# Kernel optimization log

Measured on AMD Instinct MI355X. Metric: run time of the kernel, lower is better.

## Reference

```python
import jax, jax.numpy as jnp
import numpy as np

# Model dims: batch, seq, d_model, heads, layers, vocab, ffn, max_distance
B, S, D, H, L, V, F, M = 2, 1024, 1024, 16, 6, 32000, 4096, 1024
Dh = D // H


def setup_inputs() -> dict:
    key = jax.random.key(0)
    ks = jax.random.split(key, 24)
    std = 0.02
    w = lambda k, shape: (jax.random.normal(k, shape, jnp.float32) * std)
    return {
        "tokens": jax.random.randint(ks[0], (B, S), 0, V, jnp.int32),
        "emb": w(ks[1], (V, D)),
        "Wq": w(ks[2], (L, D, D)), "bq": jnp.zeros((L, D), jnp.float32),
        "Wk": w(ks[3], (L, D, D)), "bk": jnp.zeros((L, D), jnp.float32),
        "Wv": w(ks[4], (L, D, D)), "bv": jnp.zeros((L, D), jnp.float32),
        "Wo": w(ks[5], (L, D, D)), "bo": jnp.zeros((L, D), jnp.float32),
        "rpe": w(ks[6], (L, M, Dh)),  # per-layer key-RPE embedding table
        "ln1_s": jnp.ones((L, D), jnp.float32), "ln1_b": jnp.zeros((L, D), jnp.float32),
        "ln2_s": jnp.ones((L, D), jnp.float32), "ln2_b": jnp.zeros((L, D), jnp.float32),
        "W1": w(ks[7], (L, D, F)), "b1": jnp.zeros((L, F), jnp.float32),
        "W2": w(ks[8], (L, F, D)), "b2": jnp.zeros((L, D), jnp.float32),
        "Wout": w(ks[9], (D, V)), "bout": jnp.zeros((V,), jnp.float32),
    }


def _ln(x, s, b):
    mu = jnp.mean(x, -1, keepdims=True)
    var = jnp.mean((x - mu) ** 2, -1, keepdims=True)
    return (x - mu) * jax.lax.rsqrt(var + 1e-5) * s + b


def _forward(tokens, emb, Wq, bq, Wk, bk, Wv, bv, Wo, bo, rpe,
             ln1_s, ln1_b, ln2_s, ln2_b, W1, b1, W2, b2, Wout, bout):
    x = emb[tokens]  # (B, S, D); dropout is identity at inference
    mask = jnp.tril(jnp.ones((S, S), bool))
    inv_sqrt_d = np.float32(1.0 / np.sqrt(Dh))

    def block(x, p):
        (wq, bq_, wk, bk_, wv, bv_, wo, bo_, rp,
         l1s, l1b, l2s, l2b, w1, b1_, w2, b2_) = p
        heads = lambda W, b: (x @ W + b).reshape(B, S, H, Dh).transpose(0, 2, 1, 3)
        q, k, v = heads(wq, bq_), heads(wk, bk_), heads(wv, bv_)
        qk = jnp.einsum('bhqd,bhkd->bhqk', q, k)
        # Music-Transformer skew: srel = Q @ E^T, pad-left 1, reshape, drop first row
        srel = jnp.einsum('bhqd,md->bhqm', q, rp[-S:])  # M == S, no clipping branch
        srel = jnp.pad(srel, ((0, 0), (0, 0), (0, 0), (1, 0)))
        srel = srel.reshape(B, H, S + 1, S)[:, :, 1:, :]
        logits = (qk + srel) * inv_sqrt_d
        logits = jnp.where(mask, logits, jnp.float32(-1e9))
        wgt = jax.nn.softmax(logits, axis=-1)
        o = jnp.einsum('bhqk,bhkd->bhqd', wgt, v).transpose(0, 2, 1, 3).reshape(B, S, D)
        o = o @ wo + bo_
        x2 = _ln(x + o, l1s, l1b)           # post-LN residual (attention)
        f = jax.nn.gelu(x2 @ w1 + b1_) @ w2 + b2_
        return _ln(x2 + f, l2s, l2b), None  # post-LN residual (FFN)

    x, _ = jax.lax.scan(block, x, (Wq, bq, Wk, bk, Wv, bv, Wo, bo, rpe,
                                   ln1_s, ln1_b, ln2_s, ln2_b, W1, b1, W2, b2))
    return x @ Wout + bout  # (B, S, V)


def reference(tokens, emb, Wq, bq, Wk, bk, Wv, bv, Wo, bo, rpe,
              ln1_s, ln1_b, ln2_s, ln2_b, W1, b1, W2, b2, Wout, bout):
    return _forward(tokens, emb, Wq, bq, Wk, bk, Wv, bv, Wo, bo, rpe,
                    ln1_s, ln1_b, ln2_s, ln2_b, W1, b1, W2, b2, Wout, bout)
```

## Files before the change

kernel.cpp:

```cpp
#include <hip/hip_runtime.h>
#include <hip/hip_bf16.h>
#include <cstdint>

constexpr int NB = 2, NS = 1024, ND = 1024, NH = 16, NL = 6, NV = 32000, NF = 4096, NDH = 64;

using bf16 = __hip_bfloat16;
typedef __bf16 bf16x8 __attribute__((ext_vector_type(8)));
typedef float f32x4 __attribute__((ext_vector_type(4)));

#define AS1(p) ((const __attribute__((address_space(1))) void*)(p))
#define AS3(p) ((__attribute__((address_space(3))) void*)(p))

__device__ __forceinline__ float gelu_f(float x) {
  float z = 1.5957691216057308f * (x + 0.044715f * x * x * x);
  return x / (1.f + __expf(-z));
}

template<int EP, bool HASBIAS>
__global__ __launch_bounds__(512)
void gemm256p(const bf16* __restrict__ A, const bf16* __restrict__ Bt,
              void* __restrict__ Cv, const float* __restrict__ bias,
              int K, int lda, int ldb, int ldc)
{
  const int nM = gridDim.y, nN = gridDim.x;
  const int nwg = nM * nN;
  const int bid = blockIdx.y * nN + blockIdx.x;
  const int wg = (bid & 7) * (nwg >> 3) + (bid >> 3);
  const int m0 = (wg % nM) * 256;
  const int n0 = (wg / nM) * 256;

  __shared__ char lds[131072];

  const int tid = threadIdx.x, lane = tid & 63, wid = tid >> 6;
  const int wm = (wid >> 2) * 128;
  const int wn = (wid & 3) * 64;
  const int l15 = lane & 15, g4 = lane >> 4;
  const int rdk = (g4 * 16) ^ ((l15 >> 3) << 5);

  const int srow = wid * 16 + (lane >> 2);
  const int scol = ((lane & 3) * 8) ^ (((lane >> 5) & 1) << 4);
  const bf16* gA = A  + (long)(m0 + srow) * lda + scol;
  const bf16* gB = Bt + (long)(n0 + srow) * ldb + scol;
  const long a128 = 128l * lda, b128 = 128l * ldb;

  f32x4 acc[8][4] = {};
  const int NP = K >> 5;

#define STGP(p_) do {                                                                  \
    const int s_ = (p_) & 3; const long ko_ = (long)(p_) * 32;                         \
    char* dA = lds + s_ * 32768 + wid * 1024;                                          \
    char* dB = dA + 16384;                                                             \
    __builtin_amdgcn_global_load_lds(AS1(gA + ko_),        AS3(dA),        16, 0, 0);  \
    __builtin_amdgcn_global_load_lds(AS1(gA + ko_ + a128), AS3(dA + 8192), 16, 0, 0);  \
    __builtin_amdgcn_global_load_lds(AS1(gB + ko_),        AS3(dB),        16, 0, 0);  \
    __builtin_amdgcn_global_load_lds(AS1(gB + ko_ + b128), AS3(dB + 8192), 16, 0, 0);  \
  } while (0)

#define PAIR(vm_, p_, DOSTG_) do {                                                     \
    asm volatile("s_waitcnt vmcnt(" #vm_ ")" ::: "memory");                            \
    __builtin_amdgcn_s_barrier();                                                      \
    asm volatile("" ::: "memory");                                                     \
    const char* la_ = lds + ((p_) & 3) * 32768;                                        \
    const char* lb_ = la_ + 16384;                                                     \
    bf16x8 bfr[4], af[8];                                                              \
    _Pragma("unroll") for (int j_ = 0; j_ < 4; ++j_)                                   \
      bfr[j_] = *(const bf16x8*)(lb_ + (wn + j_ * 16 + l15) * 64 + rdk);               \
    _Pragma("unroll") for (int i_ = 0; i_ < 4; ++i_)                                   \
      af[i_] = *(const bf16x8*)(la_ + (wm + i_ * 16 + l15) * 64 + rdk);                \
    __builtin_amdgcn_sched_barrier(0);                                                 \
    _Pragma("unroll") for (int i_ = 4; i_ < 8; ++i_)                                   \
      af[i_] = *(const bf16x8*)(la_ + (wm + i_ * 16 + l15) * 64 + rdk);                \
    if (DOSTG_) STGP((p_) + 3);                                                        \
    asm volatile("s_waitcnt lgkmcnt(4)" ::: "memory");                                 \
    __builtin_amdgcn_sched_barrier(0);                                                 \
    __builtin_amdgcn_s_setprio(1);                                                     \
    _Pragma("unroll") for (int i_ = 0; i_ < 4; ++i_)                                   \
      _Pragma("unroll") for (int j_ = 0; j_ < 4; ++j_)                                 \
        acc[i_][j_] = __builtin_amdgcn_mfma_f32_16x16x32_bf16(af[i_], bfr[j_], acc[i_][j_], 0, 0, 0); \
    __builtin_amdgcn_s_setprio(0);                                                     \
    asm volatile("s_waitcnt lgkmcnt(0)" ::: "memory");                                 \
    __builtin_amdgcn_sched_barrier(0);                                                 \
    __builtin_amdgcn_s_setprio(1);                                                     \
    _Pragma("unroll") for (int i_ = 4; i_ < 8; ++i_)                                   \
      _Pragma("unroll") for (int j_ = 0; j_ < 4; ++j_)                                 \
        acc[i_][j_] = __builtin_amdgcn_mfma_f32_16x16x32_bf16(af[i_], bfr[j_], acc[i_][j_], 0, 0, 0); \
    __builtin_amdgcn_s_setprio(0);                                                     \
  } while (0)

  STGP(0); STGP(1); STGP(2);
  for (int p = 0; p < NP - 3; ++p) PAIR(8, p, 1);
  PAIR(8, NP - 3, 0);
  PAIR(4, NP - 2, 0);
  PAIR(0, NP - 1, 0);
#undef PAIR
#undef STGP

  const int rq = (lane >> 4) * 4;
  #pragma unroll
  for (int i = 0; i < 8; ++i) {
    const int r0 = m0 + wm + i * 16 + rq;
    #pragma unroll
    for (int j = 0; j < 4; ++j) {
      const int c = n0 + wn + j * 16 + l15;
      float bv = 0.f;
      if constexpr (HASBIAS) bv = bias[c];
      #pragma unroll
      for (int e = 0; e < 4; ++e) {
        float v = acc[i][j][e] + bv;
        if constexpr (EP == 2) v = gelu_f(v);
        if constexpr (EP == 0) ((float*)Cv)[(long)(r0 + e) * ldc + c] = v;
        else                   ((bf16*)Cv)[(long)(r0 + e) * ldc + c] = __float2bfloat16(v);
      }
    }
  }
}

template<int EP, bool HASBIAS, int KSZ>
__global__ __launch_bounds__(256)
void gemm128_bt(const bf16* __restrict__ A, const bf16* __restrict__ Bt,
                void* __restrict__ Cv, const float* __restrict__ bias,
                int K, int lda, int ldb, int ldc, long sEP)
{
  const int nM = gridDim.y, nN = gridDim.x;
  const int nwg = nM * nN;
  const int bid = blockIdx.y * nN + blockIdx.x;
  const int qq = nwg >> 3;
  const int wg = (bid & 7) * qq + (bid >> 3);
  const int m0 = (wg % nM) * 128;
  const int n0 = (wg / nM) * 256;

  const int kLen = K / KSZ;
  const long kOff = (long)blockIdx.z * kLen;

  __shared__ char lds[73728];

  const int tid  = threadIdx.x;
  const int lane = tid & 63;
  const int wid  = tid >> 6;
  const int wn   = wid * 64;
  const int l15  = lane & 15;
  const int rdk  = ((lane >> 4) * 16) ^ ((l15 >> 3) << 5);

  const int srow = wid * 16 + (lane >> 2);
  const int scol = ((lane & 3) * 8) ^ (((lane >> 5) & 1) << 4);
  const bf16* gA = A  + (long)(m0 + srow) * lda + scol + kOff;
  const bf16* gB = Bt + (long)(n0 + srow) * ldb + scol + kOff;
  const long a64 = 64l * lda, b64 = 64l * ldb;

  f32x4 acc[8][4] = {};
  const int NT = kLen >> 5;

#define STG(t_, b_) do {                                                               \
    char* dA = lds + (b_) * 24576 + wid * 1024;                                        \
    char* dB = lds + (b_) * 24576 + 8192 + wid * 1024;                                 \
    const long ko_ = (long)(t_) * 32;                                                  \
    __builtin_amdgcn_global_load_lds(AS1(gA + ko_),           AS3(dA),         16, 0, 0); \
    __builtin_amdgcn_global_load_lds(AS1(gA + ko_ + a64),     AS3(dA + 4096),  16, 0, 0); \
    __builtin_amdgcn_global_load_lds(AS1(gB + ko_),           AS3(dB),         16, 0, 0); \
    __builtin_amdgcn_global_load_lds(AS1(gB + ko_ + b64),     AS3(dB + 4096),  16, 0, 0); \
    __builtin_amdgcn_global_load_lds(AS1(gB + ko_ + 2 * b64), AS3(dB + 8192),  16, 0, 0); \
    __builtin_amdgcn_global_load_lds(AS1(gB + ko_ + 3 * b64), AS3(dB + 12288), 16, 0, 0); \
  } while (0)

#define TBODY(cur_) do {                                                               \
    const char* la_ = lds + (cur_) * 24576;                                            \
    const char* lb_ = la_ + 8192;                                                      \
    bf16x8 bf_[4], af_[8];                                                             \
    _Pragma("unroll") for (int j_ = 0; j_ < 4; ++j_)                                   \
      bf_[j_] = *(const bf16x8*)(lb_ + (wn + j_ * 16 + l15) * 64 + rdk);               \
    _Pragma("unroll") for (int i_ = 0; i_ < 8; ++i_)                                   \
      af_[i_] = *(const bf16x8*)(la_ + (i_ * 16 + l15) * 64 + rdk);                    \
    __builtin_amdgcn_s_setprio(1);                                                     \
    _Pragma("unroll") for (int i_ = 0; i_ < 8; ++i_)                                   \
      _Pragma("unroll") for (int j_ = 0; j_ < 4; ++j_)                                 \
        acc[i_][j_] = __builtin_amdgcn_mfma_f32_16x16x32_bf16(af_[i_], bf_[j_], acc[i_][j_], 0, 0, 0); \
    __builtin_amdgcn_s_setprio(0);                                                     \
  } while (0)

  STG(0, 0); STG(1, 1);
  int cur = 0, nxt = 2;
  for (int t = 0; t < NT - 1; ++t) {
    asm volatile("s_waitcnt vmcnt(6)" ::: "memory");
    __builtin_amdgcn_s_barrier();
    asm volatile("" ::: "memory");
    if (t + 2 < NT) STG(t + 2, nxt);
    TBODY(cur);
    cur = (cur == 2) ? 0 : cur + 1;
    nxt = (nxt == 2) ? 0 : nxt + 1;
  }
  asm volatile("s_waitcnt vmcnt(0)" ::: "memory");
  __builtin_amdgcn_s_barrier();
  asm volatile("" ::: "memory");
  TBODY(cur);
#undef TBODY
#undef STG

  const int rq = (lane >> 4) * 4;
  #pragma unroll
  for (int i = 0; i < 8; ++i) {
    const int r0 = m0 + i * 16 + rq;
    #pragma unroll
    for (int j = 0; j < 4; ++j) {
      const int c = n0 + wn + j * 16 + l15;
      float bv = 0.f;
      if constexpr (HASBIAS) { if (KSZ == 1 || blockIdx.z == 0) bv = bias[c]; }
      #pragma unroll
      for (int e = 0; e < 4; ++e) {
        float v = acc[i][j][e] + bv;
        if constexpr (EP == 0) {
          float* Cz = (float*)Cv + (KSZ > 1 ? (long)blockIdx.z * sEP : 0);
          Cz[(long)(r0 + e) * ldc + c] = v;
        } else if constexpr (EP == 2) {
          ((bf16*)Cv)[(long)(r0 + e) * ldc + c] = __float2bfloat16(gelu_f(v));
        } else {
          ((bf16*)Cv)[(long)(c >> 10) * sEP + (long)(r0 + e) * ND + (c & 1023)] =
              __float2bfloat16(v);
        }
      }
    }
  }
}

template<int BN, int EP, int CZ, bool HASBIAS, int SWZ, int KS>
__global__ __launch_bounds__(256)
void gemm_bt(const bf16* __restrict__ A, const bf16* __restrict__ Bt,
             void* __restrict__ Cv, const float* __restrict__ bias,
             int M, int N, int K, int lda, int ldb, int ldc, int ZH,
             long sAb, long sAh, long sBb, long sBh, long sCb, long sCh, long sBias)
{
  constexpr int BM = 128, BK = 32;
  constexpr int WGN = (BN == 128) ? 2 : 1;
  constexpr int FM  = (BM / (4 / WGN)) / 16;
  constexpr int FN  = (BN / WGN) / 16;

  const int z  = blockIdx.z;
  const int zb = z / ZH, zh = z % ZH;
  const bf16* Ab = A + (long)zb * sAb + (long)zh * sAh;
  const bf16* Bb = Bt + (long)zb * sBb + (long)zh * sBh;

  const int m0 = blockIdx.y * BM;
  const int n0 = blockIdx.x * BN;

  if constexpr (CZ == 3) { if (m0 + n0 + BM + BN - 2 < NS - 1) return; }

  __shared__ bf16 Asm[BM * BK];
  __shared__ bf16 Bsm[BN * BK];

  const int tid  = threadIdx.x;
  const int lane = tid & 63;
  const int wid  = tid >> 6;
  const int wm = (wid / WGN) * (FM * 16);
  const int wn = (wid % WGN) * (FN * 16);
  const int l15 = lane & 15;
  const int lk8 = (lane >> 4) * 8;

  f32x4 acc[FM][FN] = {};

  const int srow = tid >> 2;
  const int scol = (tid & 3) * 8;
  const bf16* gA = Ab + (long)(m0 + srow) * lda + scol;
  const bf16* gB = Bb + (long)(n0 + srow) * ldb + scol;
  bf16* ldsA = Asm + wid * 512;
  bf16* ldsB = Bsm + wid * 512;

  for (int k0 = 0; k0 < K; k0 += BK) {
    __builtin_amdgcn_global_load_lds(AS1(gA + k0), AS3(ldsA), 16, 0, 0);
    __builtin_amdgcn_global_load_lds(AS1(gA + 64l * lda + k0), AS3(ldsA + 2048), 16, 0, 0);
    __builtin_amdgcn_global_load_lds(AS1(gB + k0), AS3(ldsB), 16, 0, 0);
    if constexpr (BN == 128)
      __builtin_amdgcn_global_load_lds(AS1(gB + 64l * ldb + k0), AS3(ldsB + 2048), 16, 0, 0);
    asm volatile("s_waitcnt vmcnt(0)" ::: "memory");
    __syncthreads();

    bf16x8 af[FM], bfr[FN];
    #pragma unroll
    for (int i = 0; i < FM; ++i)
      af[i] = *reinterpret_cast<const bf16x8*>(&Asm[(wm + i * 16 + l15) * BK + lk8]);
    #pragma unroll
    for (int j = 0; j < FN; ++j)
      bfr[j] = *reinterpret_cast<const bf16x8*>(&Bsm[(wn + j * 16 + l15) * BK + lk8]);
    #pragma unroll
    for (int i = 0; i < FM; ++i)
      #pragma unroll
      for (int j = 0; j < FN; ++j)
        acc[i][j] = __builtin_amdgcn_mfma_f32_16x16x32_bf16(af[i], bfr[j], acc[i][j], 0, 0, 0);
    __syncthreads();
  }

  const int rq = (lane >> 4) * 4;
  const long cb = (long)zb * sCb + (long)zh * sCh;
  #pragma unroll
  for (int i = 0; i < FM; ++i) {
    const int r0 = m0 + wm + i * 16 + rq;
    #pragma unroll
    for (int j = 0; j < FN; ++j) {
      const int c = n0 + wn + j * 16 + l15;
      float bv = 0.f;
      if constexpr (HASBIAS) bv = bias[(long)zb * sBias + c];
      #pragma unroll
      for (int e = 0; e < 4; ++e) {
        float v = acc[i][j][e] + bv;
        const long idx = cb + (long)(r0 + e) * ldc + c;
        if constexpr (EP == 0) ((float*)Cv)[idx] = v;
        else                   ((bf16*)Cv)[idx] = __float2bfloat16(v);
      }
    }
  }
}

__global__ __launch_bounds__(256)
void flash_attn_k(const bf16* __restrict__ qkv, const bf16* __restrict__ vt,
                  const bf16* __restrict__ qe, bf16* __restrict__ ob)
{
  const int z  = blockIdx.x;
  const int qt = 15 - blockIdx.y;
  const int b  = z >> 4, h = z & 15;
  const int q0 = qt * 64;
  const int tid  = threadIdx.x;
  const int lane = tid & 63;
  const int wid  = tid >> 6;
  const int l15  = lane & 15;
  const int g4   = lane >> 4;
  const int xk   = (l15 & 7) << 4;

  __shared__ char lds[50176];
  char* Klds = lds;
  char* Vlds = lds + 16384;
  char* Plds = lds + 32768;

  const bf16* Kg  = qkv + (long)NB * NS * ND + (long)b * NS * ND + h * 64;
  const bf16* Vg  = vt + (long)z * 64 * NS;
  const bf16* QEg = qe + (long)z * NS * NS;

  const bf16* Qrow = qkv + ((long)b * NS + q0 + wid * 16 + l15) * ND + h * 64 + g4 * 8;
  const bf16x8 qr0 = *(const bf16x8*)(Qrow);
  const bf16x8 qr1 = *(const bf16x8*)(Qrow + 32);

  const int kR = tid >> 3, kSeg = tid & 7;
  const int vD = tid >> 4, vSeg = tid & 15;
  int wKa[4], wVa[4];
  #pragma unroll
  for (int i = 0; i < 4; ++i) {
    const int r = i * 32 + kR;
    wKa[i] = (r * 128 + kSeg * 16) ^ ((r & 7) << 4);
    const int d = i * 16 + vD;
    wVa[i] = (d * 256 + vSeg * 16) ^ ((d & 7) << 4);
  }

  f32x4 aqk[8], apv[4];
  #pragma unroll
  for (int j = 0; j < 4; ++j) apv[j] = (f32x4){0.f, 0.f, 0.f, 0.f};
  float mrun[4] = {-3e38f, -3e38f, -3e38f, -3e38f};
  float lrun[4] = {0.f, 0.f, 0.f, 0.f};

  const int nk = (q0 + 191) >> 7;

  bf16x8 kr[4], vr[4];
  #pragma unroll
  for (int i = 0; i < 4; ++i) {
    kr[i] = *(const bf16x8*)(Kg + (long)(i * 32 + kR) * ND + kSeg * 8);
    vr[i] = *(const bf16x8*)(Vg + (long)(i * 16 + vD) * NS + vSeg * 8);
  }

  for (int kt = 0; kt < nk; ++kt) {
    const int k0 = kt * 128;
    __builtin_amdgcn_s_barrier();

    #pragma unroll
    for (int i = 0; i < 4; ++i) *(bf16x8*)(Klds + wKa[i]) = kr[i];
    #pragma unroll
    for (int i = 0; i < 4; ++i) *(bf16x8*)(Vlds + wVa[i]) = vr[i];

    unsigned short se[4][8];
    #pragma unroll
    for (int e = 0; e < 4; ++e) {
      const int qg = q0 + wid * 16 + g4 * 4 + e;
      const long rowb = (long)qg * NS;
      #pragma unroll
      for (int f = 0; f < 8; ++f) {
        int m = 1023 - qg + k0 + 16 * f + l15;
        m = m > 1023 ? 1023 : m;
        se[e][f] = *(const unsigned short*)(QEg + rowb + m);
      }
    }
    __builtin_amdgcn_sched_barrier(0);
    if (kt + 1 < nk) {
      const int k1 = k0 + 128;
      #pragma unroll
      for (int i = 0; i < 4; ++i) {
        kr[i] = *(const bf16x8*)(Kg + (long)(k1 + i * 32 + kR) * ND + kSeg * 8);
        vr[i] = *(const bf16x8*)(Vg + (long)(i * 16 + vD) * NS + k1 + vSeg * 8);
      }
    }
    asm volatile("s_waitcnt lgkmcnt(0)" ::: "memory");
    __builtin_amdgcn_sched_barrier(0);
    __builtin_amdgcn_s_barrier();

    #pragma unroll
    for (int f = 0; f < 8; ++f) aqk[f] = (f32x4){0.f, 0.f, 0.f, 0.f};
    {
      const int ko0 = g4 * 16;
      #pragma unroll
      for (int f = 0; f < 8; ++f) {
        bf16x8 bb = *(const bf16x8*)(Klds + (((16 * f + l15) * 128 + ko0) ^ xk));
        aqk[f] = __builtin_amdgcn_mfma_f32_16x16x32_bf16(qr0, bb, aqk[f], 0, 0, 0);
      }
      const int ko1 = 64 + g4 * 16;
      #pragma unroll
      for (int f = 0; f < 8; ++f) {
        bf16x8 bb = *(const bf16x8*)(Klds + (((16 * f + l15) * 128 + ko1) ^ xk));
        aqk[f] = __builtin_amdgcn_mfma_f32_16x16x32_bf16(qr1, bb, aqk[f], 0, 0, 0);
      }
    }

    float ps[4][8];
    float scl[4];
    #pragma unroll
    for (int e = 0; e < 4; ++e) {
      const int qg = q0 + wid * 16 + g4 * 4 + e;
      float s[8];
      float mx = mrun[e];
      #pragma unroll
      for (int f = 0; f < 8; ++f) {
        const int kg = k0 + 16 * f + l15;
        const float sv = __uint_as_float((unsigned)se[e][f] << 16);
        const float t = (aqk[f][e] + sv) * 0.125f;
        s[f] = (kg <= qg) ? t : -1e30f;
        mx = fmaxf(mx, s[f]);
      }
      #pragma unroll
      for (int o = 1; o < 16; o <<= 1) mx = fmaxf(mx, __shfl_xor(mx, o));
      const float sc_ = __expf(mrun[e] - mx);
      float ls = 0.f;
      #pragma unroll
      for (int f = 0; f < 8; ++f) { const float p = __expf(s[f] - mx); ps[e][f] = p; ls += p; }
      #pragma unroll
      for (int o = 1; o < 16; o <<= 1) ls += __shfl_xor(ls, o);
      lrun[e] = lrun[e] * sc_ + ls;
      mrun[e] = mx;
      scl[e] = sc_;
    }
    #pragma unroll
    for (int fd = 0; fd < 4; ++fd)
      #pragma unroll
      for (int e = 0; e < 4; ++e) apv[fd][e] *= scl[e];

    #pragma unroll
    for (int e = 0; e < 4; ++e) {
      char* pr = Plds + (wid * 16 + g4 * 4 + e) * 272 + l15 * 2;
      #pragma unroll
      for (int f = 0; f < 8; ++f)
        *(bf16*)(pr + f * 32) = __float2bfloat16(ps[e][f]);
    }
    asm volatile("s_waitcnt lgkmcnt(0)" ::: "memory");
    __builtin_amdgcn_sched_barrier(0);

    #pragma unroll
    for (int ks = 0; ks < 4; ++ks) {
      const int ko = (ks * 32 + g4 * 8) * 2;
      bf16x8 a = *(const bf16x8*)(Plds + (wid * 16 + l15) * 272 + ko);
      #pragma unroll
      for (int fd = 0; fd < 4; ++fd) {
        bf16x8 bb = *(const bf16x8*)(Vlds + (((16 * fd + l15) * 256 + ko) ^ xk));
        apv[fd] = __builtin_amdgcn_mfma_f32_16x16x32_bf16(a, bb, apv[fd], 0, 0, 0);
      }
    }
  }

  #pragma unroll
  for (int e = 0; e < 4; ++e) {
    const float rl = 1.f / lrun[e];
    const int qg = q0 + wid * 16 + g4 * 4 + e;
    bf16* orow = ob + ((long)b * NS + qg) * ND + h * 64;
    #pragma unroll
    for (int fd = 0; fd < 4; ++fd)
      orow[16 * fd + l15] = __float2bfloat16(apv[fd][e] * rl);
  }
}

__global__ void transpose64_k(const float* __restrict__ in, bf16* __restrict__ out,
                              int R, int C, long inZ, long outZ) {
  __shared__ float t[64][65];
  const float* ip = in + (long)blockIdx.z * inZ;
  bf16* op = out + (long)blockIdx.z * outZ;
  const int c0 = blockIdx.x * 64, r0 = blockIdx.y * 64;
  const int tid = threadIdx.x;
  const int lr = tid >> 4;
  const int lc = (tid & 15) * 4;
  #pragma unroll
  for (int i = 0; i < 4; ++i) {
    const float4 v = *(const float4*)(ip + (long)(r0 + lr + 16 * i) * C + c0 + lc);
    t[lr + 16 * i][lc]     = v.x;
    t[lr + 16 * i][lc + 1] = v.y;
    t[lr + 16 * i][lc + 2] = v.z;
    t[lr + 16 * i][lc + 3] = v.w;
  }
  __syncthreads();
  #pragma unroll
  for (int i = 0; i < 4; ++i) {
    const int oc = lr + 16 * i;
    ushort4 u;
    bf16 h0 = __float2bfloat16(t[lc][oc]);
    bf16 h1 = __float2bfloat16(t[lc + 1][oc]);
    bf16 h2 = __float2bfloat16(t[lc + 2][oc]);
    bf16 h3 = __float2bfloat16(t[lc + 3][oc]);
    u.x = *(unsigned short*)&h0; u.y = *(unsigned short*)&h1;
    u.z = *(unsigned short*)&h2; u.w = *(unsigned short*)&h3;
    *(ushort4*)(op + (long)(c0 + oc) * R + r0 + lc) = u;
  }
}

__global__ void transpose_v_k(const bf16* __restrict__ v, bf16* __restrict__ vt) {
  __shared__ bf16 t[32][33];
  const int z = blockIdx.z, b = z >> 4, h = z & 15;
  const bf16* ip = v + (long)b * NS * ND + h * 64;
  bf16* op = vt + (long)z * 64 * NS;
  const int s0 = blockIdx.x * 32, d0 = blockIdx.y * 32;
  const int tx = threadIdx.x, ty = threadIdx.y;
  #pragma unroll
  for (int i = 0; i < 4; ++i)
    t[ty * 4 + i][tx] = ip[(long)(s0 + ty * 4 + i) * ND + d0 + tx];
  __syncthreads();
  #pragma unroll
  for (int i = 0; i < 4; ++i)
    op[(long)(d0 + ty * 4 + i) * NS + s0 + tx] = t[tx][ty * 4 + i];
}

__global__ void cvt_bf16_k(const float* __restrict__ in, bf16* __restrict__ out, int n) {
  int i = blockIdx.x * 256 + threadIdx.x;
  if (i < n) out[i] = __float2bfloat16(in[i]);
}

__global__ void pack3_k(const float* __restrict__ a, const float* __restrict__ b,
                        const float* __restrict__ c, float* __restrict__ out) {
  int i = blockIdx.x * 256 + threadIdx.x;
  if (i >= NL * 3 * ND) return;
  int d = i % ND, r = (i / ND) % 3, l = i / (3 * ND);
  const float* src = (r == 0) ? a : ((r == 1) ? b : c);
  out[i] = src[l * ND + d];
}

__global__ void embed_k(const int* __restrict__ tok, const float* __restrict__ emb,
                        float* __restrict__ x, bf16* __restrict__ xb) {
  const int row = blockIdx.x;
  const int t = tok[row];
  const float4 val = ((const float4*)(emb + (long)t * ND))[threadIdx.x];
  ((float4*)(x + (long)row * ND))[threadIdx.x] = val;
  bf16* xp = xb + (long)row * ND + threadIdx.x * 4;
  xp[0] = __float2bfloat16(val.x); xp[1] = __float2bfloat16(val.y);
  xp[2] = __float2bfloat16(val.z); xp[3] = __float2bfloat16(val.w);
}

__global__ void resid_ln_k(float* __restrict__ x, const float* __restrict__ g,
                           long gs,
                           const float* __restrict__ s, const float* __restrict__ b,
                           bf16* __restrict__ xb) {
  const int row = blockIdx.x, tid = threadIdx.x;
  const float4 xv = ((const float4*)(x + (long)row * ND))[tid];
  const float4 ga = ((const float4*)(g + (long)row * ND))[tid];
  const float4 gb = ((const float4*)(g + gs + (long)row * ND))[tid];
  const float4 gc = ((const float4*)(g + 2 * gs + (long)row * ND))[tid];
  const float4 gd = ((const float4*)(g + 3 * gs + (long)row * ND))[tid];
  float h0 = xv.x + ga.x + gb.x + gc.x + gd.x;
  float h1 = xv.y + ga.y + gb.y + gc.y + gd.y;
  float h2 = xv.z + ga.z + gb.z + gc.z + gd.z;
  float h3 = xv.w + ga.w + gb.w + gc.w + gd.w;
  float ls = h0 + h1 + h2 + h3;
  __shared__ float red[8];
  #pragma unroll
  for (int o = 32; o; o >>= 1) ls += __shfl_xor(ls, o);
  const int lane = tid & 63, wid = tid >> 6;
  if (lane == 0) red[wid] = ls;
  __syncthreads();
  const float mu = (red[0] + red[1] + red[2] + red[3]) * (1.f / ND);
  const float d0 = h0 - mu, d1 = h1 - mu, d2 = h2 - mu, d3 = h3 - mu;
  float lv = d0 * d0 + d1 * d1 + d2 * d2 + d3 * d3;
  #pragma unroll
  for (int o = 32; o; o >>= 1) lv += __shfl_xor(lv, o);
  if (lane == 0) red[4 + wid] = lv;
  __syncthreads();
  const float rs = rsqrtf((red[4] + red[5] + red[6] + red[7]) * (1.f / ND) + 1e-5f);
  const float4 sv = ((const float4*)s)[tid];
  const float4 bv = ((const float4*)b)[tid];
  const float y0 = d0 * rs * sv.x + bv.x, y1 = d1 * rs * sv.y + bv.y;
  const float y2 = d2 * rs * sv.z + bv.z, y3 = d3 * rs * sv.w + bv.w;
  ((float4*)(x + (long)row * ND))[tid] = make_float4(y0, y1, y2, y3);
  bf16* xp = xb + (long)row * ND + tid * 4;
  xp[0] = __float2bfloat16(y0); xp[1] = __float2bfloat16(y1);
  xp[2] = __float2bfloat16(y2); xp[3] = __float2bfloat16(y3);
}

extern "C" void kernel_launch(void* const* d_in, const int* in_sizes, int n_in,
                              void* d_out, int out_size, void* d_ws, size_t ws_size,
                              hipStream_t stream) {
  const int*   tokens = (const int*)d_in[0];
  const float* emb  = (const float*)d_in[1];
  const float* Wq   = (const float*)d_in[2];
  const float* bq   = (const float*)d_in[3];
  const float* Wk   = (const float*)d_in[4];
  const float* bk   = (const float*)d_in[5];
  const float* Wv   = (const float*)d_in[6];
  const float* bv   = (const float*)d_in[7];
  const float* Wo   = (const float*)d_in[8];
  const float* bo   = (const float*)d_in[9];
  const float* rpe  = (const float*)d_in[10];
  const float* ln1s = (const float*)d_in[11];
  const float* ln1b = (const float*)d_in[12];
  const float* ln2s = (const float*)d_in[13];
  const float* ln2b = (const float*)d_in[14];
  const float* W1   = (const float*)d_in[15];
  const float* b1   = (const float*)d_in[16];
  const float* W2   = (const float*)d_in[17];
  const float* b2   = (const float*)d_in[18];
  const float* Wout = (const float*)d_in[19];
  const float* bout = (const float*)d_in[20];
  float* out = (float*)d_out;

  char* wsb = (char*)d_ws;
  size_t off = 0;
  auto take = [&](size_t bytes) -> void* {
    void* r = wsb + off;
    off = (off + bytes + 255) & ~(size_t)255;
    return r;
  };
  bf16*  wqkvT = (bf16*)take((size_t)NL * 3 * ND * ND * 2);
  bf16*  woT   = (bf16*)take((size_t)NL * ND * ND * 2);
  bf16*  w1T   = (bf16*)take((size_t)NL * NF * ND * 2);
  bf16*  w2T   = (bf16*)take((size_t)NL * ND * NF * 2);
  bf16*  woutT = (bf16*)take((size_t)NV * ND * 2);
  bf16*  rpeb  = (bf16*)take((size_t)NL * NS * NDH * 2);
  float* qkvb  = (float*)take((size_t)NL * 3 * ND * 4);
  float* x     = (float*)take((size_t)NB * NS * ND * 4);
  bf16*  xb    = (bf16*)take((size_t)NB * NS * ND * 2);
  bf16*  qkv   = (bf16*)take((size_t)3 * NB * NS * ND * 2);
  bf16*  vt    = (bf16*)take((size_t)NB * NS * ND * 2);
  bf16*  ob    = (bf16*)take((size_t)NB * NS * ND * 2);
  float* g     = (float*)take((size_t)4 * NB * NS * ND * 4);
  bf16*  hbuf  = (bf16*)take((size_t)NB * NS * NF * 2);
  bf16*  qe    = (bf16*)take((size_t)NB * NH * NS * NS * 2 + 4096);
  (void)in_sizes; (void)n_in; (void)out_size; (void)ws_size;

  const long gStride = (long)NB * NS * ND;

  transpose64_k<<<dim3(ND/64, ND/64, NL), 256, 0, stream>>>(Wq, wqkvT,                   ND, ND, (long)ND*ND, (long)3*ND*ND);
  transpose64_k<<<dim3(ND/64, ND/64, NL), 256, 0, stream>>>(Wk, wqkvT + (size_t)ND*ND,   ND, ND, (long)ND*ND, (long)3*ND*ND);
  transpose64_k<<<dim3(ND/64, ND/64, NL), 256, 0, stream>>>(Wv, wqkvT + (size_t)2*ND*ND, ND, ND, (long)ND*ND, (long)3*ND*ND);
  transpose64_k<<<dim3(ND/64, ND/64, NL), 256, 0, stream>>>(Wo, woT,                     ND, ND, (long)ND*ND, (long)ND*ND);
  transpose64_k<<<dim3(NF/64, ND/64, NL), 256, 0, stream>>>(W1, w1T,                     ND, NF, (long)ND*NF, (long)NF*ND);
  transpose64_k<<<dim3(ND/64, NF/64, NL), 256, 0, stream>>>(W2, w2T,                     NF, ND, (long)NF*ND, (long)ND*NF);
  transpose64_k<<<dim3(NV/64, ND/64, 1),  256, 0, stream>>>(Wout, woutT,                 ND, NV, 0, 0);
  cvt_bf16_k<<<(NL*NS*NDH + 255)/256, 256, 0, stream>>>(rpe, rpeb, NL*NS*NDH);
  pack3_k<<<(NL*3*ND + 255)/256, 256, 0, stream>>>(bq, bk, bv, qkvb);
  embed_k<<<NB*NS, 256, 0, stream>>>(tokens, emb, x, xb);

  const dim3 tb(32, 8);
  for (int l = 0; l < NL; ++l) {
    gemm128_bt<3, true, 1><<<dim3(3*ND/256, NB*NS/128), 256, 0, stream>>>(
        xb, wqkvT + (size_t)l*3*ND*ND, qkv, qkvb + (size_t)l*3*ND,
        ND, ND, ND, ND, gStride);
    transpose_v_k<<<dim3(NS/32, 2, NB*NH), tb, 0, stream>>>(qkv + (size_t)2*NB*NS*ND, vt);
    gemm_bt<128, 1, 3, false, 0, 0><<<dim3(NS/128, NS/128, NB*NH), 256, 0, stream>>>(
        qkv, rpeb + (size_t)l*NS*NDH, qe, nullptr,
        NS, NS, NDH, ND, NDH, NS, NH,
        (long)NS*ND, 64, 0, 0, (long)NH*NS*NS, (long)NS*NS, 0);
    flash_attn_k<<<dim3(NB*NH, 16), 256, 0, stream>>>(qkv, vt, qe, ob);
    gemm128_bt<0, true, 4><<<dim3(ND/256, NB*NS/128, 4), 256, 0, stream>>>(
        ob, woT + (size_t)l*ND*ND, g, bo + (size_t)l*ND, ND, ND, ND, ND, gStride);
    resid_ln_k<<<NB*NS, 256, 0, stream>>>(x, g, gStride,
        ln1s + (size_t)l*ND, ln1b + (size_t)l*ND, xb);
    gemm128_bt<2, true, 1><<<dim3(NF/256, NB*NS/128), 256, 0, stream>>>(
        xb, w1T + (size_t)l*NF*ND, hbuf, b1 + (size_t)l*NF, ND, ND, ND, NF, 0);
    gemm128_bt<0, true, 4><<<dim3(ND/256, NB*NS/128, 4), 256, 0, stream>>>(
        hbuf, w2T + (size_t)l*ND*NF, g, b2 + (size_t)l*ND, NF, NF, NF, ND, gStride);
    resid_ln_k<<<NB*NS, 256, 0, stream>>>(x, g, gStride,
        ln2s + (size_t)l*ND, ln2b + (size_t)l*ND, xb);
  }
  gemm256p<0, true><<<dim3(NV/256, NB*NS/256), 512, 0, stream>>>(
      xb, woutT, out, bout, ND, ND, ND, NV);
}
```

Measured before the change: 1.355 ms.

## Replace direct global-to-LDS loads with register-staged double-buffered GEMM pipeline

The GEMM mainloop no longer uses global_load_lds to fill LDS stages directly. Tiles are now loaded into registers two iterations ahead, then written to a swizzled LDS slot after the barrier, with two register sets ping-ponged. The aim is to let the compiler's own waitcnt tracking hide global latency and to apply the XOR swizzle at the LDS write side. It costs extra VGPRs and explicit ds_write instructions per iteration, and it relies on the compiler placing vmcnt waits correctly.

```diff
diff --git a/kernel.cpp b/kernel.cpp
--- a/kernel.cpp
+++ b/kernel.cpp
@@ -38,28 +38,34 @@
   const int rdk = (g4 * 16) ^ ((l15 >> 3) << 5);
 
   const int srow = wid * 16 + (lane >> 2);
-  const int scol = ((lane & 3) * 8) ^ (((lane >> 5) & 1) << 4);
+  const int scol = (lane & 3) * 8;
   const bf16* gA = A  + (long)(m0 + srow) * lda + scol;
   const bf16* gB = Bt + (long)(n0 + srow) * ldb + scol;
   const long a128 = 128l * lda, b128 = 128l * ldb;
+  const int wb = srow * 64 + (((lane & 3) * 16) ^ (((lane >> 5) & 1) << 5));
 
   f32x4 acc[8][4] = {};
   const int NP = K >> 5;
 
-#define STGP(p_) do {                                                                  \
-    const int s_ = (p_) & 3; const long ko_ = (long)(p_) * 32;                         \
-    char* dA = lds + s_ * 32768 + wid * 1024;                                          \
-    char* dB = dA + 16384;                                                             \
-    __builtin_amdgcn_global_load_lds(AS1(gA + ko_),        AS3(dA),        16, 0, 0);  \
-    __builtin_amdgcn_global_load_lds(AS1(gA + ko_ + a128), AS3(dA + 8192), 16, 0, 0);  \
-    __builtin_amdgcn_global_load_lds(AS1(gB + ko_),        AS3(dB),        16, 0, 0);  \
-    __builtin_amdgcn_global_load_lds(AS1(gB + ko_ + b128), AS3(dB + 8192), 16, 0, 0);  \
+#define LOADC(p_, SAlo, SAhi, SBlo, SBhi) do {                                         \
+    const long ko_ = (long)(p_) * 32;                                                  \
+    SAlo = *(const bf16x8*)(gA + ko_); SAhi = *(const bf16x8*)(gA + ko_ + a128);       \
+    SBlo = *(const bf16x8*)(gB + ko_); SBhi = *(const bf16x8*)(gB + ko_ + b128);       \
   } while (0)
 
-#define PAIR(vm_, p_, DOSTG_) do {                                                     \
-    asm volatile("s_waitcnt vmcnt(" #vm_ ")" ::: "memory");                            \
+#define WRITEC(p_, SAlo, SAhi, SBlo, SBhi) do {                                        \
+    char* wbase_ = lds + (((p_) & 3) * 32768);                                         \
+    *(bf16x8*)(wbase_ + wb)          = SAlo;                                           \
+    *(bf16x8*)(wbase_ + 8192 + wb)   = SAhi;                                           \
+    *(bf16x8*)(wbase_ + 16384 + wb)  = SBlo;                                           \
+    *(bf16x8*)(wbase_ + 24576 + wb)  = SBhi;                                           \
+  } while (0)
+
+#define PAIRB(p_, SAlo, SAhi, SBlo, SBhi, DOW_, DOL_) do {                             \
     __builtin_amdgcn_s_barrier();                                                      \
     asm volatile("" ::: "memory");                                                     \
+    if (DOW_) WRITEC((p_) + 2, SAlo, SAhi, SBlo, SBhi);                                \
+    __builtin_amdgcn_sched_barrier(0);                                                 \
     const char* la_ = lds + ((p_) & 3) * 32768;                                        \
     const char* lb_ = la_ + 16384;                                                     \
     bf16x8 bfr[4], af[8];                                                              \
@@ -70,8 +76,10 @@
     __builtin_amdgcn_sched_barrier(0);                                                 \
     _Pragma("unroll") for (int i_ = 4; i_ < 8; ++i_)                                   \
       af[i_] = *(const bf16x8*)(la_ + (wm + i_ * 16 + l15) * 64 + rdk);                \
-    if (DOSTG_) STGP((p_) + 3);                                                        \
+    __builtin_amdgcn_sched_barrier(0);                                                 \
     asm volatile("s_waitcnt lgkmcnt(4)" ::: "memory");                                 \
+    __builtin_amdgcn_sched_barrier(0);                                                 \
+    if (DOL_) LOADC((p_) + 4, SAlo, SAhi, SBlo, SBhi);                                 \
     __builtin_amdgcn_sched_barrier(0);                                                 \
     __builtin_amdgcn_s_setprio(1);                                                     \
     _Pragma("unroll") for (int i_ = 0; i_ < 4; ++i_)                                   \
@@ -87,13 +95,25 @@
     __builtin_amdgcn_s_setprio(0);                                                     \
   } while (0)
 
-  STGP(0); STGP(1); STGP(2);
-  for (int p = 0; p < NP - 3; ++p) PAIR(8, p, 1);
-  PAIR(8, NP - 3, 0);
-  PAIR(4, NP - 2, 0);
-  PAIR(0, NP - 1, 0);
-#undef PAIR
-#undef STGP
+  bf16x8 A0lo, A0hi, B0lo, B0hi, A1lo, A1hi, B1lo, B1hi;
+  LOADC(0, A0lo, A0hi, B0lo, B0hi);
+  LOADC(1, A1lo, A1hi, B1lo, B1hi);
+  WRITEC(0, A0lo, A0hi, B0lo, B0hi);
+  LOADC(2, A0lo, A0hi, B0lo, B0hi);
+  WRITEC(1, A1lo, A1hi, B1lo, B1hi);
+  LOADC(3, A1lo, A1hi, B1lo, B1hi);
+  asm volatile("s_waitcnt lgkmcnt(0)" ::: "memory");
+
+  int p = 0;
+  for (; p < NP - 2; p += 2) {
+    PAIRB(p,     A0lo, A0hi, B0lo, B0hi, true, (p + 4 < NP));
+    PAIRB(p + 1, A1lo, A1hi, B1lo, B1hi, true, (p + 5 < NP));
+  }
+  PAIRB(NP - 2, A0lo, A0hi, B0lo, B0hi, false, false);
+  PAIRB(NP - 1, A1lo, A1hi, B1lo, B1hi, false, false);
+#undef PAIRB
+#undef WRITEC
+#undef LOADC
 
   const int rq = (lane >> 4) * 4;
   #pragma unroll
```

After: 1.366 ms. About the same (+0.8%).

## Replace 256x256 output-projection GEMM with 128x256 double-buffered variant

Applied to the files above, without the earlier changes.

The final vocabulary-projection GEMM moves from a 512-thread 256x256 tile with a 4-stage LDS pipeline to a 256-thread 128x256 tile with a 2-stage double buffer using 48KB of LDS. Each wave now covers all 128 rows and 64 columns. The pipeline adds a second barrier before restaging into the buffer just read. The smaller LDS footprint and block size should allow more resident workgroups and more blocks across CUs. In exchange, per-tile reuse of B drops and the pipeline is shallower, so load latency is less hidden.

```diff
diff --git a/kernel.cpp b/kernel.cpp
--- a/kernel.cpp
+++ b/kernel.cpp
@@ -17,88 +17,82 @@
 }
 
 template<int EP, bool HASBIAS>
-__global__ __launch_bounds__(512)
-void gemm256p(const bf16* __restrict__ A, const bf16* __restrict__ Bt,
-              void* __restrict__ Cv, const float* __restrict__ bias,
-              int K, int lda, int ldb, int ldc)
+__global__ __launch_bounds__(256)
+void gemm128v2(const bf16* __restrict__ A, const bf16* __restrict__ Bt,
+               void* __restrict__ Cv, const float* __restrict__ bias,
+               int K, int lda, int ldb, int ldc)
 {
   const int nM = gridDim.y, nN = gridDim.x;
   const int nwg = nM * nN;
   const int bid = blockIdx.y * nN + blockIdx.x;
   const int wg = (bid & 7) * (nwg >> 3) + (bid >> 3);
-  const int m0 = (wg % nM) * 256;
+  const int m0 = (wg % nM) * 128;
   const int n0 = (wg / nM) * 256;
 
-  __shared__ char lds[131072];
-
-  const int tid = threadIdx.x, lane = tid & 63, wid = tid >> 6;
-  const int wm = (wid >> 2) * 128;
-  const int wn = (wid & 3) * 64;
-  const int l15 = lane & 15, g4 = lane >> 4;
-  const int rdk = (g4 * 16) ^ ((l15 >> 3) << 5);
+  __shared__ char lds[49152];
+
+  const int tid  = threadIdx.x;
+  const int lane = tid & 63;
+  const int wid  = tid >> 6;
+  const int wn   = wid * 64;
+  const int l15  = lane & 15;
+  const int rdk  = ((lane >> 4) * 16) ^ ((l15 >> 3) << 5);
 
   const int srow = wid * 16 + (lane >> 2);
   const int scol = ((lane & 3) * 8) ^ (((lane >> 5) & 1) << 4);
   const bf16* gA = A  + (long)(m0 + srow) * lda + scol;
   const bf16* gB = Bt + (long)(n0 + srow) * ldb + scol;
-  const long a128 = 128l * lda, b128 = 128l * ldb;
+  const long a64 = 64l * lda, b64 = 64l * ldb;
 
   f32x4 acc[8][4] = {};
-  const int NP = K >> 5;
-
-#define STGP(p_) do {                                                                  \
-    const int s_ = (p_) & 3; const long ko_ = (long)(p_) * 32;                         \
-    char* dA = lds + s_ * 32768 + wid * 1024;                                          \
-    char* dB = dA + 16384;                                                             \
-    __builtin_amdgcn_global_load_lds(AS1(gA + ko_),        AS3(dA),        16, 0, 0);  \
-    __builtin_amdgcn_global_load_lds(AS1(gA + ko_ + a128), AS3(dA + 8192), 16, 0, 0);  \
-    __builtin_amdgcn_global_load_lds(AS1(gB + ko_),        AS3(dB),        16, 0, 0);  \
-    __builtin_amdgcn_global_load_lds(AS1(gB + ko_ + b128), AS3(dB + 8192), 16, 0, 0);  \
+  const int NT = K >> 5;
+
+#define STG(t_, b_) do {                                                               \
+    char* dA = lds + (b_) * 24576 + wid * 1024;                                        \
+    char* dB = lds + (b_) * 24576 + 8192 + wid * 1024;                                 \
+    const long ko_ = (long)(t_) * 32;                                                  \
+    __builtin_amdgcn_global_load_lds(AS1(gA + ko_),           AS3(dA),         16, 0, 0); \
+    __builtin_amdgcn_global_load_lds(AS1(gA + ko_ + a64),     AS3(dA + 4096),  16, 0, 0); \
+    __builtin_amdgcn_global_load_lds(AS1(gB + ko_),           AS3(dB),         16, 0, 0); \
+    __builtin_amdgcn_global_load_lds(AS1(gB + ko_ + b64),     AS3(dB + 4096),  16, 0, 0); \
+    __builtin_amdgcn_global_load_lds(AS1(gB + ko_ + 2 * b64), AS3(dB + 8192),  16, 0, 0); \
+    __builtin_amdgcn_global_load_lds(AS1(gB + ko_ + 3 * b64), AS3(dB + 12288), 16, 0, 0); \
   } while (0)
 
-#define PAIR(vm_, p_, DOSTG_) do {                                                     \
+#define TILE(vm_, t_, DOSTG_) do {                                                     \
     asm volatile("s_waitcnt vmcnt(" #vm_ ")" ::: "memory");                            \
     __builtin_amdgcn_s_barrier();                                                      \
     asm volatile("" ::: "memory");                                                     \
-    const char* la_ = lds + ((p_) & 3) * 32768;                                        \
-    const char* lb_ = la_ + 16384;                                                     \
+    const char* la_ = lds + ((t_) & 1) * 24576;                                        \
+    const char* lb_ = la_ + 8192;                                                      \
     bf16x8 bfr[4], af[8];                                                              \
     _Pragma("unroll") for (int j_ = 0; j_ < 4; ++j_)                                   \
       bfr[j_] = *(const bf16x8*)(lb_ + (wn + j_ * 16 + l15) * 64 + rdk);               \
-    _Pragma("unroll") for (int i_ = 0; i_ < 4; ++i_)                                   \
-      af[i_] = *(const bf16x8*)(la_ + (wm + i_ * 16 + l15) * 64 + rdk);                \
-    __builtin_amdgcn_sched_barrier(0);                                                 \
-    _Pragma("unroll") for (int i_ = 4; i_ < 8; ++i_)                                   \
-      af[i_] = *(const bf16x8*)(la_ + (wm + i_ * 16 + l15) * 64 + rdk);                \
-    if (DOSTG_) STGP((p_) + 3);                                                        \
-    asm volatile("s_waitcnt lgkmcnt(4)" ::: "memory");                                 \
-    __builtin_amdgcn_sched_barrier(0);                                                 \
-    __builtin_amdgcn_s_setprio(1);                                                     \
-    _Pragma("unroll") for (int i_ = 0; i_ < 4; ++i_)                                   \
-      _Pragma("unroll") for (int j_ = 0; j_ < 4; ++j_)                                 \
-        acc[i_][j_] = __builtin_amdgcn_mfma_f32_16x16x32_bf16(af[i_], bfr[j_], acc[i_][j_], 0, 0, 0); \
-    __builtin_amdgcn_s_setprio(0);                                                     \
+    _Pragma("unroll") for (int i_ = 0; i_ < 8; ++i_)                                   \
+      af[i_] = *(const bf16x8*)(la_ + (i_ * 16 + l15) * 64 + rdk);                     \
     asm volatile("s_waitcnt lgkmcnt(0)" ::: "memory");                                 \
     __builtin_amdgcn_sched_barrier(0);                                                 \
+    __builtin_amdgcn_s_barrier();                                                      \
+    asm volatile("" ::: "memory");                                                     \
+    if (DOSTG_) STG((t_) + 2, (t_) & 1);                                               \
     __builtin_amdgcn_s_setprio(1);                                                     \
-    _Pragma("unroll") for (int i_ = 4; i_ < 8; ++i_)                                   \
+    _Pragma("unroll") for (int i_ = 0; i_ < 8; ++i_)                                   \
       _Pragma("unroll") for (int j_ = 0; j_ < 4; ++j_)                                 \
         acc[i_][j_] = __builtin_amdgcn_mfma_f32_16x16x32_bf16(af[i_], bfr[j_], acc[i_][j_], 0, 0, 0); \
     __builtin_amdgcn_s_setprio(0);                                                     \
   } while (0)
 
-  STGP(0); STGP(1); STGP(2);
-  for (int p = 0; p < NP - 3; ++p) PAIR(8, p, 1);
-  PAIR(8, NP - 3, 0);
-  PAIR(4, NP - 2, 0);
-  PAIR(0, NP - 1, 0);
-#undef PAIR
-#undef STGP
+  STG(0, 0); STG(1, 1);
+  for (int t = 0; t < NT - 2; ++t) TILE(6, t, true);
+  TILE(6, NT - 2, false);
+  TILE(0, NT - 1, false);
+#undef TILE
+#undef STG
 
   const int rq = (lane >> 4) * 4;
   #pragma unroll
   for (int i = 0; i < 8; ++i) {
-    const int r0 = m0 + wm + i * 16 + rq;
+    const int r0 = m0 + i * 16 + rq;
     #pragma unroll
     for (int j = 0; j < 4; ++j) {
       const int c = n0 + wn + j * 16 + l15;
@@ -675,6 +669,6 @@
     resid_ln_k<<<NB*NS, 256, 0, stream>>>(x, g, gStride,
         ln2s + (size_t)l*ND, ln2b + (size_t)l*ND, xb);
   }
-  gemm256p<0, true><<<dim3(NV/256, NB*NS/256), 512, 0, stream>>>(
+  gemm128v2<0, true><<<dim3(NV/256, NB*NS/128), 256, 0, stream>>>(
       xb, woutT, out, bout, ND, ND, ND, NV);
 }
```

Result: slower. 1.436 ms (+5.9%).
